# Kernel tuning notes

Measured on AMD Instinct MI355X. Metric: run time of the kernel, lower is better.

## Reference

```python
import jax, jax.numpy as jnp
import numpy as np

W_SIZE = 8
SHIFT = 4
HEADS = 8
EPS = 1e-5


def _layernorm(x, w, b):
    mu = jnp.mean(x, axis=-1, keepdims=True)
    var = jnp.var(x, axis=-1, keepdims=True)
    return (x - mu) * jax.lax.rsqrt(var + EPS) * w + b


def setup_inputs() -> dict:
    key = jax.random.key(0)
    ks = jax.random.split(key, 8)
    B, C, L = 8, 256, 16384
    s = lambda fan: 1.0 / np.sqrt(fan)
    return {
        "x": jax.random.normal(ks[0], (B, C, L), jnp.float32),
        "norm1_w": jnp.ones((C,), jnp.float32),
        "norm1_b": jnp.zeros((C,), jnp.float32),
        "norm2_w": jnp.ones((C,), jnp.float32),
        "norm2_b": jnp.zeros((C,), jnp.float32),
        "qkv_w": jax.random.normal(ks[1], (C, 3 * C), jnp.float32) * s(C),
        "proj_w": jax.random.normal(ks[2], (C, C), jnp.float32) * s(C),
        "proj_b": jnp.zeros((C,), jnp.float32),
        "ff1_w": jax.random.normal(ks[3], (C, 4 * C), jnp.float32) * s(C),
        "ff1_b": jnp.zeros((4 * C,), jnp.float32),
        "ff2_w": jax.random.normal(ks[4], (4 * C, C), jnp.float32) * s(4 * C),
        "ff2_b": jnp.zeros((C,), jnp.float32),
    }


def _window_attn(xt, qkv_w, proj_w, proj_b):
    # xt: (B, L, C); L assumed divisible by W_SIZE (pad path unused for chosen L)
    B, L, C = xt.shape
    W, H = W_SIZE, HEADS
    D = C // H
    scale = D ** (-0.5)
    if SHIFT:
        xt = jnp.roll(xt, -SHIFT, axis=1)
    n_win = L // W
    xw = xt.reshape(B, n_win, W, C)
    qkv = xw @ qkv_w                      # (B, n, W, 3C)
    q, k, v = jnp.split(qkv, 3, axis=-1)
    def heads(t):
        return t.reshape(B, n_win, W, H, D).transpose(0, 1, 3, 2, 4)  # (B,n,H,W,D)
    q, k, v = heads(q), heads(k), heads(v)
    attn = jnp.einsum('bnhid,bnhjd->bnhij', q, k) * scale
    attn = jax.nn.softmax(attn, axis=-1)
    out = jnp.einsum('bnhij,bnhjd->bnhid', attn, v)
    out = out.transpose(0, 1, 3, 2, 4).reshape(B, n_win, W, C)
    out = out @ proj_w + proj_b
    out = out.reshape(B, L, C)
    if SHIFT:
        out = jnp.roll(out, SHIFT, axis=1)
    return out


def reference(x, norm1_w, norm1_b, norm2_w, norm2_b, qkv_w, proj_w, proj_b,
              ff1_w, ff1_b, ff2_w, ff2_b):
    xt = jnp.transpose(x, (0, 2, 1))  # (B, L, C)
    xt = xt + _window_attn(_layernorm(xt, norm1_w, norm1_b), qkv_w, proj_w, proj_b)
    h = jax.nn.gelu(_layernorm(xt, norm2_w, norm2_b) @ ff1_w + ff1_b, approximate=False)
    xt = xt + (h @ ff2_w + ff2_b)
    return jnp.transpose(xt, (0, 2, 1))  # (B, C, L)
```

## Files before the change

kernel.cpp:

```cpp
#include <hip/hip_runtime.h>
#include <hip/hip_bf16.h>

#define C_ 256
#define L_ 16384
#define CL_ (C_*L_)

typedef unsigned int u32;
typedef unsigned short u16;
typedef __bf16 bf16_t;
typedef bf16_t bf16x8 __attribute__((ext_vector_type(8)));
typedef float f32x4 __attribute__((ext_vector_type(4)));

__device__ __forceinline__ float bf2f(u16 v){ return __builtin_bit_cast(float, ((u32)v)<<16); }
__device__ __forceinline__ u16 f2bf(float f){
  bf16_t h = (bf16_t)f;
  return __builtin_bit_cast(u16, h);
}
__device__ __forceinline__ u32 pack2(float a, float b){
  return (u32)f2bf(a) | ((u32)f2bf(b)<<16);
}

#define AST 528
#define HST 272
#define CST 136
#define OST 68

__global__ void wpack_kernel(const float* __restrict__ qkvw, const float* __restrict__ projw,
                             const float* __restrict__ f1w, const float* __restrict__ f2w,
                             u16* __restrict__ pq, u16* __restrict__ pp,
                             u16* __restrict__ p1, u16* __restrict__ p2)
{
  int bid = blockIdx.x, tid = threadIdx.x;
  const float* src; u16* dst; int stride, n, k;
  if (bid < 96){
    int f = bid*256 + tid;
    int l = f & 63, nt = (f>>6) & 15, kk = f>>10;
    int s = kk>>3, ks = kk&7;
    stride = 768; src = qkvw;
    n = s*256 + nt*16 + (l&15);
    k = ks*32 + ((l>>4)<<3);
    dst = pq + (size_t)s*65536 + ((size_t)(ks*16 + nt)*64 + l)*8;
  } else if (bid < 128){
    int f = (bid-96)*256 + tid;
    int l = f & 63, nt = (f>>6) & 15, ks = f>>10;
    stride = 256; src = projw;
    n = nt*16 + (l&15);
    k = ks*32 + ((l>>4)<<3);
    dst = pp + ((size_t)(ks*16 + nt)*64 + l)*8;
  } else if (bid < 256){
    int f = (bid-128)*256 + tid;
    int l = f & 63, nt = (f>>6) & 15, kk = f>>10;
    int c2 = kk>>3, ks = kk&7;
    stride = 1024; src = f1w;
    n = c2*256 + nt*16 + (l&15);
    k = ks*32 + ((l>>4)<<3);
    dst = p1 + (size_t)c2*65536 + ((size_t)(ks*16 + nt)*64 + l)*8;
  } else {
    int f = (bid-256)*256 + tid;
    int l = f & 63, nt = (f>>6) & 15, ks = f>>10;
    stride = 256; src = f2w;
    n = nt*16 + (l&15);
    k = ks*32 + ((l>>4)<<3);
    dst = p2 + ((size_t)(ks*16 + nt)*64 + l)*8;
  }
  u16 v[8];
  #pragma unroll
  for (int j = 0; j < 8; ++j) v[j] = f2bf(src[(size_t)(k+j)*stride + n]);
  uint4 o;
  o.x = (u32)v[0] | ((u32)v[1]<<16);
  o.y = (u32)v[2] | ((u32)v[3]<<16);
  o.z = (u32)v[4] | ((u32)v[5]<<16);
  o.w = (u32)v[6] | ((u32)v[7]<<16);
  *(uint4*)dst = o;
}

__device__ __forceinline__ void gemmP(const u16* Abase, const u16* __restrict__ pk,
                                      int l, int ntb, f32x4 acc[4][2])
{
  const char* ab = (const char*)Abase + (l&15)*AST + ((l>>4)<<4);
  const u16* bp = pk + ((size_t)ntb*64 + l)*8;
  #pragma unroll
  for (int ks = 0; ks < 8; ++ks){
    const u16* bk = bp + (size_t)ks*8192;
    bf16x8 b0 = *(const bf16x8*)(bk);
    bf16x8 b1 = *(const bf16x8*)(bk + 512);
    bf16x8 a[4];
    #pragma unroll
    for (int m = 0; m < 4; ++m)
      a[m] = *(const bf16x8*)(ab + m*(16*AST) + ks*64);
    #pragma unroll
    for (int m = 0; m < 4; ++m){
      acc[m][0] = __builtin_amdgcn_mfma_f32_16x16x32_bf16(a[m], b0, acc[m][0], 0, 0, 0);
      acc[m][1] = __builtin_amdgcn_mfma_f32_16x16x32_bf16(a[m], b1, acc[m][1], 0, 0, 0);
    }
  }
}
#define ZERO_ACC(A) { _Pragma("unroll") for (int m_ = 0; m_ < 4; ++m_){ A[m_][0] = (f32x4){0,0,0,0}; A[m_][1] = (f32x4){0,0,0,0}; } }

__device__ __forceinline__ void gemmP3(const u16* Abase, const u16* __restrict__ pkq,
                                       int l, int ntb,
                                       f32x4 aq[4][2], f32x4 ak[4][2], f32x4 av[4][2])
{
  const char* ab = (const char*)Abase + (l&15)*AST + ((l>>4)<<4);
  const u16* bq = pkq + ((size_t)ntb*64 + l)*8;
  #pragma unroll
  for (int ks = 0; ks < 8; ++ks){
    const u16* bkq = bq + (size_t)ks*8192;
    bf16x8 q0 = *(const bf16x8*)(bkq);
    bf16x8 q1 = *(const bf16x8*)(bkq + 512);
    bf16x8 k0 = *(const bf16x8*)(bkq + 65536);
    bf16x8 k1 = *(const bf16x8*)(bkq + 65536 + 512);
    bf16x8 v0 = *(const bf16x8*)(bkq + 131072);
    bf16x8 v1 = *(const bf16x8*)(bkq + 131072 + 512);
    bf16x8 a[4];
    #pragma unroll
    for (int m = 0; m < 4; ++m)
      a[m] = *(const bf16x8*)(ab + m*(16*AST) + ks*64);
    #pragma unroll
    for (int m = 0; m < 4; ++m){
      aq[m][0] = __builtin_amdgcn_mfma_f32_16x16x32_bf16(a[m], q0, aq[m][0], 0, 0, 0);
      aq[m][1] = __builtin_amdgcn_mfma_f32_16x16x32_bf16(a[m], q1, aq[m][1], 0, 0, 0);
      ak[m][0] = __builtin_amdgcn_mfma_f32_16x16x32_bf16(a[m], k0, ak[m][0], 0, 0, 0);
      ak[m][1] = __builtin_amdgcn_mfma_f32_16x16x32_bf16(a[m], k1, ak[m][1], 0, 0, 0);
      av[m][0] = __builtin_amdgcn_mfma_f32_16x16x32_bf16(a[m], v0, av[m][0], 0, 0, 0);
      av[m][1] = __builtin_amdgcn_mfma_f32_16x16x32_bf16(a[m], v1, av[m][1], 0, 0, 0);
    }
  }
}

__device__ __forceinline__ void gemmF(const u16* Abase, const u16* __restrict__ pk,
                                      int l, int ntb, f32x4 acc[4][2])
{
  #pragma unroll
  for (int ks = 0; ks < 8; ++ks){
    bf16x8 b0 = *(const bf16x8*)(pk + ((size_t)(ks*16 + ntb    )*64 + l)*8);
    bf16x8 b1 = *(const bf16x8*)(pk + ((size_t)(ks*16 + ntb + 1)*64 + l)*8);
    int k0 = ks*32;
    bf16x8 a[4];
    #pragma unroll
    for (int m = 0; m < 4; ++m){
      int t = m*16 + (l & 15);
      int off = t*512 + ((2*(k0 + ((l>>4)<<3))) ^ ((t&7)<<4));
      a[m] = *(const bf16x8*)((const char*)Abase + off);
    }
    #pragma unroll
    for (int m = 0; m < 4; ++m){
      acc[m][0] = __builtin_amdgcn_mfma_f32_16x16x32_bf16(a[m], b0, acc[m][0], 0, 0, 0);
      acc[m][1] = __builtin_amdgcn_mfma_f32_16x16x32_bf16(a[m], b1, acc[m][1], 0, 0, 0);
    }
  }
}

__launch_bounds__(512, 2)
__global__ void swin_attn_kernel(const float* __restrict__ x,
                                 const float* __restrict__ n1w, const float* __restrict__ n1b,
                                 const u16* __restrict__ pkq, const u16* __restrict__ pkp,
                                 const float* __restrict__ projb,
                                 u16* __restrict__ xt1g, float* __restrict__ statsg)
{
  __shared__ char smem[73216];
  u16* Buf1 = (u16*)smem;
  char* Buf2 = smem + 33792;
  float* redF = (float*)(smem + 68608);
  float* statsF = redF + 1024;

  const int tid = threadIdx.x;
  const int w = tid >> 6;
  const int l = tid & 63;
  const int bb = blockIdx.x >> 8;
  const int blkl = blockIdx.x & 255;
  const int l0 = blkl*64 + 4;
  const float* xb = x + (size_t)bb*CL_;
  const int ntb = w*2;

  const int q4 = tid & 15, cg = tid >> 4;
  int lq = l0 + 4*q4; if (lq >= L_) lq -= L_;
  u32 praw[4][4];
  {
    float4 xr[8];
    float s1[4] = {0.f,0.f,0.f,0.f};
    float s2[4] = {0.f,0.f,0.f,0.f};
    #pragma unroll
    for (int ci = 0; ci < 8; ++ci){
      int c = cg*8 + ci;
      float4 d = *(const float4*)(xb + (size_t)c*L_ + lq);
      xr[ci] = d;
      s1[0]+=d.x; s2[0]+=d.x*d.x;  s1[1]+=d.y; s2[1]+=d.y*d.y;
      s1[2]+=d.z; s2[2]+=d.z*d.z;  s1[3]+=d.w; s2[3]+=d.w*d.w;
    }
    #pragma unroll
    for (int off = 16; off < 64; off <<= 1){
      #pragma unroll
      for (int jj = 0; jj < 4; ++jj){
        s1[jj] += __shfl_xor(s1[jj], off);
        s2[jj] += __shfl_xor(s2[jj], off);
      }
    }
    if (l < 16){
      #pragma unroll
      for (int jj = 0; jj < 4; ++jj){
        redF[w*64 + 4*l + jj] = s1[jj];
        redF[512 + w*64 + 4*l + jj] = s2[jj];
      }
    }
    __syncthreads();
    if (tid < 64){
      float a = 0.f, b2 = 0.f;
      #pragma unroll
      for (int ww = 0; ww < 8; ++ww){ a += redF[ww*64 + tid]; b2 += redF[512 + ww*64 + tid]; }
      float mu = a * (1.f/256.f);
      float var = fmaxf(b2 * (1.f/256.f) - mu*mu, 0.f);
      statsF[2*tid] = mu;
      statsF[2*tid+1] = rsqrtf(var + 1e-5f);
    }
    __syncthreads();
    #pragma unroll
    for (int jj = 0; jj < 4; ++jj){
      int t = 4*q4 + jj;
      float mu = statsF[2*t], rs = statsF[2*t+1];
      u32 aw[4];
      #pragma unroll
      for (int cp = 0; cp < 4; ++cp){
        int c0c = cg*8 + 2*cp;
        float v0 = ((const float*)&xr[2*cp])[jj];
        float v1 = ((const float*)&xr[2*cp+1])[jj];
        aw[cp] = pack2((v0-mu)*rs*n1w[c0c] + n1b[c0c], (v1-mu)*rs*n1w[c0c+1] + n1b[c0c+1]);
        praw[jj][cp] = pack2(v0, v1);
      }
      *(uint4*)((char*)Buf1 + t*AST + cg*16) = make_uint4(aw[0],aw[1],aw[2],aw[3]);
    }
  }
  __syncthreads();

  f32x4 aq[4][2], ak[4][2], av[4][2];
  ZERO_ACC(aq); ZERO_ACC(ak); ZERO_ACC(av);
  gemmP3(Buf1, pkq, l, ntb, aq, ak, av);

  #pragma unroll
  for (int m = 0; m < 4; ++m)
    #pragma unroll
    for (int n2 = 0; n2 < 2; ++n2)
      #pragma unroll
      for (int jj = 0; jj < 4; ++jj){
        int t = m*16 + ((l>>4)<<2) + jj;
        int c = (w<<5) + (n2<<4) + (l&15);
        *(u16*)(Buf2 + t*AST + 2*c) = f2bf(ak[m][n2][jj]);
      }
  __syncthreads();

  const int hh = (tid >> 3) & 7, rr = tid & 7;
  const int tq = w*8 + rr;
  u32 kr[16];
  #pragma unroll
  for (int g = 0; g < 4; ++g){
    uint4 dk = *(const uint4*)(Buf2 + tq*AST + hh*64 + 16*g);
    kr[g*4+0] = dk.x; kr[g*4+1] = dk.y; kr[g*4+2] = dk.z; kr[g*4+3] = dk.w;
  }
  __syncthreads();

  #pragma unroll
  for (int m = 0; m < 4; ++m)
    #pragma unroll
    for (int n2 = 0; n2 < 2; ++n2)
      #pragma unroll
      for (int jj = 0; jj < 4; ++jj){
        int t = m*16 + ((l>>4)<<2) + jj;
        int c = (w<<5) + (n2<<4) + (l&15);
        *(u16*)(Buf2 + t*AST + 2*c) = f2bf(aq[m][n2][jj]);
      }
  __syncthreads();

  float pr[8];
  {
    float qf[32];
    #pragma unroll
    for (int g = 0; g < 4; ++g){
      uint4 dq = *(const uint4*)(Buf2 + tq*AST + hh*64 + 16*g);
      qf[g*8+0] = bf2f((u16)dq.x); qf[g*8+1] = bf2f((u16)(dq.x>>16));
      qf[g*8+2] = bf2f((u16)dq.y); qf[g*8+3] = bf2f((u16)(dq.y>>16));
      qf[g*8+4] = bf2f((u16)dq.z); qf[g*8+5] = bf2f((u16)(dq.z>>16));
      qf[g*8+6] = bf2f((u16)dq.w); qf[g*8+7] = bf2f((u16)(dq.w>>16));
    }
    float s[8];
    #pragma unroll
    for (int j = 0; j < 8; ++j){
      float dot = 0.f;
      #pragma unroll
      for (int reg = 0; reg < 16; ++reg){
        u32 kj = (u32)__shfl((int)kr[reg], j, 8);
        dot += qf[2*reg]   * bf2f((u16)kj);
        dot += qf[2*reg+1] * bf2f((u16)(kj>>16));
      }
      s[j] = dot * 0.17677669529663687f;
    }
    float mx = s[0];
    #pragma unroll
    for (int j = 1; j < 8; ++j) mx = fmaxf(mx, s[j]);
    float sum = 0.f;
    #pragma unroll
    for (int j = 0; j < 8; ++j){ pr[j] = __expf(s[j]-mx); sum += pr[j]; }
    float inv = 1.0f / sum;
    #pragma unroll
    for (int j = 0; j < 8; ++j) pr[j] *= inv;
  }
  __syncthreads();

  #pragma unroll
  for (int m = 0; m < 4; ++m)
    #pragma unroll
    for (int n2 = 0; n2 < 2; ++n2)
      #pragma unroll
      for (int jj = 0; jj < 4; ++jj){
        int t = m*16 + ((l>>4)<<2) + jj;
        int c = (w<<5) + (n2<<4) + (l&15);
        *(u16*)(Buf2 + t*AST + 2*c) = f2bf(av[m][n2][jj]);
      }
  #pragma unroll
  for (int jj = 0; jj < 4; ++jj){
    int t = 4*q4 + jj;
    *(uint4*)((char*)Buf1 + t*AST + cg*16) =
        make_uint4(praw[jj][0], praw[jj][1], praw[jj][2], praw[jj][3]);
  }
  __syncthreads();

  {
    u32 vr[16];
    #pragma unroll
    for (int g = 0; g < 4; ++g){
      uint4 dv = *(const uint4*)(Buf2 + tq*AST + hh*64 + 16*g);
      vr[g*4+0] = dv.x; vr[g*4+1] = dv.y; vr[g*4+2] = dv.z; vr[g*4+3] = dv.w;
    }
    float of[32];
    #pragma unroll
    for (int d = 0; d < 32; ++d) of[d] = 0.f;
    #pragma unroll
    for (int j = 0; j < 8; ++j){
      float pj = pr[j];
      #pragma unroll
      for (int reg = 0; reg < 16; ++reg){
        u32 vj = (u32)__shfl((int)vr[reg], j, 8);
        of[2*reg]   += pj*bf2f((u16)vj);
        of[2*reg+1] += pj*bf2f((u16)(vj>>16));
      }
    }
    #pragma unroll
    for (int g = 0; g < 4; ++g){
      uint4 o;
      o.x = pack2(of[g*8+0], of[g*8+1]);
      o.y = pack2(of[g*8+2], of[g*8+3]);
      o.z = pack2(of[g*8+4], of[g*8+5]);
      o.w = pack2(of[g*8+6], of[g*8+7]);
      *(uint4*)(Buf2 + tq*AST + hh*64 + 16*g) = o;
    }
  }
  __syncthreads();

  {
    f32x4 acc[4][2]; ZERO_ACC(acc);
    gemmP((const u16*)Buf2, pkp, l, ntb, acc);
    __syncthreads();
    #pragma unroll
    for (int m = 0; m < 4; ++m)
      #pragma unroll
      for (int n2 = 0; n2 < 2; ++n2)
        #pragma unroll
        for (int jj = 0; jj < 4; ++jj){
          int t = m*16 + ((l>>4)<<2) + jj;
          int c = (w<<5) + (n2<<4) + (l&15);
          float rv = bf2f(*(const u16*)((char*)Buf1 + t*AST + 2*c));
          float v = acc[m][n2][jj] + projb[c] + rv;
          *(u16*)(Buf2 + c*CST + 2*t) = f2bf(v);
        }
  }
  __syncthreads();

  {
    float a = 0.f, b2 = 0.f;
    #pragma unroll
    for (int ci = 0; ci < 32; ++ci){
      int c = (w<<5) + ci;
      float v = bf2f(*(const u16*)(Buf2 + c*CST + 2*l));
      a += v; b2 += v*v;
    }
    redF[w*64 + l] = a;
    redF[512 + w*64 + l] = b2;
  }
  u16* xo = xt1g + (size_t)bb*CL_;
  #pragma unroll
  for (int ii = 0; ii < 8; ++ii){
    int id = tid + ii*512;
    int c = id >> 4, qd = id & 15;
    int lw = l0 + 4*qd; if (lw >= L_) lw -= L_;
    uint2 dd = *(const uint2*)(Buf2 + c*CST + 8*qd);
    *(uint2*)(xo + (size_t)c*L_ + lw) = dd;
  }
  __syncthreads();
  if (tid < 64){
    float a = 0.f, b2 = 0.f;
    #pragma unroll
    for (int ww = 0; ww < 8; ++ww){ a += redF[ww*64 + tid]; b2 += redF[512 + ww*64 + tid]; }
    float mu = a * (1.f/256.f);
    float var = fmaxf(b2 * (1.f/256.f) - mu*mu, 0.f);
    float2 st; st.x = mu; st.y = rsqrtf(var + 1e-5f);
    *(float2*)(statsg + (size_t)(bb*16384 + blkl*64 + tid)*2) = st;
  }
}

__launch_bounds__(512, 4)
__global__ void swin_ff_kernel(const u16* __restrict__ xt1g, const float* __restrict__ statsg,
                               const float* __restrict__ n2w, const float* __restrict__ n2b,
                               const u16* __restrict__ pk1, const float* __restrict__ f1b,
                               const u16* __restrict__ pk2, const float* __restrict__ f2b,
                               float* __restrict__ out)
{
  __shared__ char smem[51200];
  u16* Buf1 = (u16*)smem;
  char* BufH = smem + 33792;

  const int tid = threadIdx.x;
  const int w = tid >> 6;
  const int l = tid & 63;
  const int bb = blockIdx.x >> 8;
  const int blkl = blockIdx.x & 255;
  const int l0 = blkl*64 + 4;
  const u16* xi = xt1g + (size_t)bb*CL_;

  const int q4 = tid & 15, cg = tid >> 4;
  int lq = l0 + 4*q4; if (lq >= L_) lq -= L_;
  {
    u32 xl[8][2];
    #pragma unroll
    for (int ci = 0; ci < 8; ++ci){
      int c = cg*8 + ci;
      uint2 dd = *(const uint2*)(xi + (size_t)c*L_ + lq);
      xl[ci][0] = dd.x; xl[ci][1] = dd.y;
    }
    #pragma unroll
    for (int jj = 0; jj < 4; ++jj){
      int t = 4*q4 + jj;
      float2 st = *(const float2*)(statsg + (size_t)(bb*16384 + blkl*64 + t)*2);
      float mu = st.x, rs = st.y;
      u32 aw[4];
      #pragma unroll
      for (int cp = 0; cp < 4; ++cp){
        int c0c = cg*8 + 2*cp;
        float v0 = bf2f((u16)(xl[2*cp  ][jj>>1] >> (16*(jj&1))));
        float v1 = bf2f((u16)(xl[2*cp+1][jj>>1] >> (16*(jj&1))));
        aw[cp] = pack2((v0-mu)*rs*n2w[c0c] + n2b[c0c], (v1-mu)*rs*n2w[c0c+1] + n2b[c0c+1]);
      }
      *(uint4*)((char*)Buf1 + t*AST + cg*16) = make_uint4(aw[0],aw[1],aw[2],aw[3]);
    }
  }
  __syncthreads();

  f32x4 acc2[4][2]; ZERO_ACC(acc2);
  const char* ab1 = (const char*)Buf1 + (l&15)*AST + ((l>>4)<<4);
  const char* abh = BufH + (l&15)*HST + ((l>>4)<<4);
  #pragma unroll 1
  for (int j = 0; j < 8; ++j){
    f32x4 acc1[4];
    #pragma unroll
    for (int m = 0; m < 4; ++m) acc1[m] = (f32x4){0,0,0,0};
    const u16* p1 = pk1 + (size_t)(j>>1)*65536;
    const int ntf = ((j&1)<<3) + w;
    const u16* bp1 = p1 + ((size_t)ntf*64 + l)*8;
    #pragma unroll
    for (int ks = 0; ks < 8; ++ks){
      bf16x8 b = *(const bf16x8*)(bp1 + (size_t)ks*8192);
      #pragma unroll
      for (int m = 0; m < 4; ++m){
        bf16x8 a = *(const bf16x8*)(ab1 + m*(16*AST) + ks*64);
        acc1[m] = __builtin_amdgcn_mfma_f32_16x16x32_bf16(a, b, acc1[m], 0, 0, 0);
      }
    }
    __syncthreads();
    #pragma unroll
    for (int m = 0; m < 4; ++m)
      #pragma unroll
      for (int jj = 0; jj < 4; ++jj){
        int t = m*16 + ((l>>4)<<2) + jj;
        int cp_ = (w<<4) + (l&15);
        float xv = acc1[m][jj] + f1b[j*128 + cp_];
        float u = xv*(0.79788456f + 0.035677408f*xv*xv);
        float g = xv / (1.f + __expf(-2.f*u));
        *(u16*)(BufH + t*HST + 2*cp_) = f2bf(g);
      }
    __syncthreads();
    const u16* bp2 = pk2 + ((size_t)(4*j*16 + 2*w)*64 + l)*8;
    #pragma unroll
    for (int ks2 = 0; ks2 < 4; ++ks2){
      const u16* bk = bp2 + (size_t)ks2*8192;
      bf16x8 b0 = *(const bf16x8*)(bk);
      bf16x8 b1 = *(const bf16x8*)(bk + 512);
      bf16x8 a[4];
      #pragma unroll
      for (int m = 0; m < 4; ++m)
        a[m] = *(const bf16x8*)(abh + m*(16*HST) + ks2*64);
      #pragma unroll
      for (int m = 0; m < 4; ++m){
        acc2[m][0] = __builtin_amdgcn_mfma_f32_16x16x32_bf16(a[m], b0, acc2[m][0], 0, 0, 0);
        acc2[m][1] = __builtin_amdgcn_mfma_f32_16x16x32_bf16(a[m], b1, acc2[m][1], 0, 0, 0);
      }
    }
  }

  float* OutF = (float*)smem;
  float* ob = out + (size_t)bb*CL_;
  #pragma unroll
  for (int n2p = 0; n2p < 2; ++n2p){
    __syncthreads();
    #pragma unroll
    for (int m = 0; m < 4; ++m)
      #pragma unroll
      for (int jj = 0; jj < 4; ++jj){
        int t = m*16 + ((l>>4)<<2) + jj;
        int c = (w<<5) + (n2p<<4) + (l&15);
        int row = (w<<4) + (l&15);
        float v = acc2[m][n2p][jj] + f2b[c];
        OutF[row*OST + t] = v;
      }
    __syncthreads();
    #pragma unroll
    for (int ii = 0; ii < 4; ++ii){
      int id = tid + ii*512;
      int row = id >> 4, qd = id & 15;
      int cg_ = ((row>>4)<<5) + (n2p<<4) + (row&15);
      int lw = l0 + 4*qd; if (lw >= L_) lw -= L_;
      float4 vv = *(const float4*)(OutF + row*OST + 4*qd);
      uint2 rr2 = *(const uint2*)(xi + (size_t)cg_*L_ + lw);
      vv.x += bf2f((u16)rr2.x);  vv.y += bf2f((u16)(rr2.x>>16));
      vv.z += bf2f((u16)rr2.y);  vv.w += bf2f((u16)(rr2.y>>16));
      *(float4*)(ob + (size_t)cg_*L_ + lw) = vv;
    }
  }
}

__launch_bounds__(512, 2)
__global__ void swin_fused_kernel(const float* __restrict__ x,
                                  const float* __restrict__ n1w, const float* __restrict__ n1b,
                                  const float* __restrict__ n2w, const float* __restrict__ n2b,
                                  const u16* __restrict__ pkq, const u16* __restrict__ pkp,
                                  const float* __restrict__ projb,
                                  const u16* __restrict__ pk1, const float* __restrict__ f1b,
                                  const u16* __restrict__ pk2, const float* __restrict__ f2b,
                                  float* __restrict__ out)
{
  __shared__ u16 smem[35072];
  u16* Buf1 = smem;
  u16* Buf2 = smem + 16384;
  float* redF   = (float*)(smem + 32768);
  float* statsF = redF + 1024;

  const int tid = threadIdx.x;
  const int w = tid >> 6;
  const int l = tid & 63;
  const int bb = blockIdx.x >> 8;
  const int blkl = blockIdx.x & 255;
  const int l0 = blkl*64 + 4;
  const float* xb = x + (size_t)bb*CL_;
  const int ntb = w*2;

  const int q4 = tid & 15, cg = tid >> 4;
  int lq = l0 + 4*q4; if (lq >= L_) lq -= L_;
  float4 xr[8];
  float s1[4] = {0.f,0.f,0.f,0.f};
  float s2[4] = {0.f,0.f,0.f,0.f};
  #pragma unroll
  for (int ci = 0; ci < 8; ++ci){
    int c = cg*8 + ci;
    float4 d = *(const float4*)(xb + (size_t)c*L_ + lq);
    xr[ci] = d;
    s1[0]+=d.x; s2[0]+=d.x*d.x;  s1[1]+=d.y; s2[1]+=d.y*d.y;
    s1[2]+=d.z; s2[2]+=d.z*d.z;  s1[3]+=d.w; s2[3]+=d.w*d.w;
  }
  #pragma unroll
  for (int off = 16; off < 64; off <<= 1){
    #pragma unroll
    for (int jj = 0; jj < 4; ++jj){
      s1[jj] += __shfl_xor(s1[jj], off);
      s2[jj] += __shfl_xor(s2[jj], off);
    }
  }
  if (l < 16){
    #pragma unroll
    for (int jj = 0; jj < 4; ++jj){
      redF[w*64 + 4*l + jj] = s1[jj];
      redF[512 + w*64 + 4*l + jj] = s2[jj];
    }
  }
  __syncthreads();
  if (tid < 64){
    float a = 0.f, b2 = 0.f;
    #pragma unroll
    for (int ww = 0; ww < 8; ++ww){ a += redF[ww*64 + tid]; b2 += redF[512 + ww*64 + tid]; }
    float mu = a * (1.f/256.f);
    float var = fmaxf(b2 * (1.f/256.f) - mu*mu, 0.f);
    statsF[2*tid] = mu;
    statsF[2*tid+1] = rsqrtf(var + 1e-5f);
  }
  __syncthreads();

  u32 praw[4][4];
  #pragma unroll
  for (int jj = 0; jj < 4; ++jj){
    int t = 4*q4 + jj;
    float mu = statsF[2*t], rs = statsF[2*t+1];
    u32 aw[4];
    #pragma unroll
    for (int cp = 0; cp < 4; ++cp){
      int c0c = cg*8 + 2*cp;
      float v0 = ((const float*)&xr[2*cp])[jj];
      float v1 = ((const float*)&xr[2*cp+1])[jj];
      aw[cp] = pack2((v0-mu)*rs*n1w[c0c] + n1b[c0c], (v1-mu)*rs*n1w[c0c+1] + n1b[c0c+1]);
      praw[jj][cp] = pack2(v0, v1);
    }
    *(uint4*)((char*)Buf1 + t*512 + ((cg*16) ^ ((t&7)<<4))) = make_uint4(aw[0],aw[1],aw[2],aw[3]);
  }
  __syncthreads();

  {
    f32x4 acc[4][2]; ZERO_ACC(acc);
    gemmF(Buf1, pkq + 65536, l, ntb, acc);
    #pragma unroll
    for (int m = 0; m < 4; ++m)
      #pragma unroll
      for (int n2 = 0; n2 < 2; ++n2)
        #pragma unroll
        for (int jj = 0; jj < 4; ++jj){
          int t = m*16 + ((l>>4)<<2) + jj;
          int c = (w<<5) + (n2<<4) + (l&15);
          *(u16*)((char*)Buf2 + t*512 + ((2*c) ^ ((t&7)<<4))) = f2bf(acc[m][n2][jj]);
        }
  }
  __syncthreads();

  const int hh = (tid >> 3) & 7, rr = tid & 7;
  const int tq = w*8 + rr;
  u32 kr[16];
  #pragma unroll
  for (int g = 0; g < 4; ++g){
    uint4 dk = *(const uint4*)((char*)Buf2 + tq*512 + ((hh*64 + 16*g) ^ ((tq&7)<<4)));
    kr[g*4+0] = dk.x; kr[g*4+1] = dk.y; kr[g*4+2] = dk.z; kr[g*4+3] = dk.w;
  }
  __syncthreads();

  {
    f32x4 acc[4][2]; ZERO_ACC(acc);
    gemmF(Buf1, pkq, l, ntb, acc);
    #pragma unroll
    for (int m = 0; m < 4; ++m)
      #pragma unroll
      for (int n2 = 0; n2 < 2; ++n2)
        #pragma unroll
        for (int jj = 0; jj < 4; ++jj){
          int t = m*16 + ((l>>4)<<2) + jj;
          int c = (w<<5) + (n2<<4) + (l&15);
          *(u16*)((char*)Buf2 + t*512 + ((2*c) ^ ((t&7)<<4))) = f2bf(acc[m][n2][jj]);
        }
  }
  __syncthreads();

  float pr[8];
  {
    float qf[32];
    #pragma unroll
    for (int g = 0; g < 4; ++g){
      uint4 dq = *(const uint4*)((char*)Buf2 + tq*512 + ((hh*64 + 16*g) ^ ((tq&7)<<4)));
      qf[g*8+0] = bf2f((u16)dq.x); qf[g*8+1] = bf2f((u16)(dq.x>>16));
      qf[g*8+2] = bf2f((u16)dq.y); qf[g*8+3] = bf2f((u16)(dq.y>>16));
      qf[g*8+4] = bf2f((u16)dq.z); qf[g*8+5] = bf2f((u16)(dq.z>>16));
      qf[g*8+6] = bf2f((u16)dq.w); qf[g*8+7] = bf2f((u16)(dq.w>>16));
    }
    float s[8];
    #pragma unroll
    for (int j = 0; j < 8; ++j){
      float dot = 0.f;
      #pragma unroll
      for (int reg = 0; reg < 16; ++reg){
        u32 kj = (u32)__shfl((int)kr[reg], j, 8);
        dot += qf[2*reg]   * bf2f((u16)kj);
        dot += qf[2*reg+1] * bf2f((u16)(kj>>16));
      }
      s[j] = dot * 0.17677669529663687f;
    }
    float mx = s[0];
    #pragma unroll
    for (int j = 1; j < 8; ++j) mx = fmaxf(mx, s[j]);
    float sum = 0.f;
    #pragma unroll
    for (int j = 0; j < 8; ++j){ pr[j] = __expf(s[j]-mx); sum += pr[j]; }
    float inv = 1.0f / sum;
    #pragma unroll
    for (int j = 0; j < 8; ++j) pr[j] *= inv;
  }
  __syncthreads();

  {
    f32x4 acc[4][2]; ZERO_ACC(acc);
    gemmF(Buf1, pkq + 131072, l, ntb, acc);
    __syncthreads();
    #pragma unroll
    for (int m = 0; m < 4; ++m)
      #pragma unroll
      for (int n2 = 0; n2 < 2; ++n2)
        #pragma unroll
        for (int jj = 0; jj < 4; ++jj){
          int t = m*16 + ((l>>4)<<2) + jj;
          int c = (w<<5) + (n2<<4) + (l&15);
          *(u16*)((char*)Buf2 + t*512 + ((2*c) ^ ((t&7)<<4))) = f2bf(acc[m][n2][jj]);
        }
    #pragma unroll
    for (int jj = 0; jj < 4; ++jj){
      int t = 4*q4 + jj;
      *(uint4*)((char*)Buf1 + t*512 + ((cg*16) ^ ((t&7)<<4))) =
          make_uint4(praw[jj][0], praw[jj][1], praw[jj][2], praw[jj][3]);
    }
  }
  __syncthreads();

  {
    u32 vr[16];
    #pragma unroll
    for (int g = 0; g < 4; ++g){
      uint4 dv = *(const uint4*)((char*)Buf2 + tq*512 + ((hh*64 + 16*g) ^ ((tq&7)<<4)));
      vr[g*4+0] = dv.x; vr[g*4+1] = dv.y; vr[g*4+2] = dv.z; vr[g*4+3] = dv.w;
    }
    float of[32];
    #pragma unroll
    for (int d = 0; d < 32; ++d) of[d] = 0.f;
    #pragma unroll
    for (int j = 0; j < 8; ++j){
      float pj = pr[j];
      #pragma unroll
      for (int reg = 0; reg < 16; ++reg){
        u32 vj = (u32)__shfl((int)vr[reg], j, 8);
        of[2*reg]   += pj*bf2f((u16)vj);
        of[2*reg+1] += pj*bf2f((u16)(vj>>16));
      }
    }
    #pragma unroll
    for (int g = 0; g < 4; ++g){
      uint4 o;
      o.x = pack2(of[g*8+0], of[g*8+1]);
      o.y = pack2(of[g*8+2], of[g*8+3]);
      o.z = pack2(of[g*8+4], of[g*8+5]);
      o.w = pack2(of[g*8+6], of[g*8+7]);
      *(uint4*)((char*)Buf2 + tq*512 + ((hh*64 + 16*g) ^ ((tq&7)<<4))) = o;
    }
  }
  __syncthreads();

  u32 xt1p[4][2][2];
  {
    f32x4 acc[4][2]; ZERO_ACC(acc);
    gemmF(Buf2, pkp, l, ntb, acc);
    __syncthreads();
    #pragma unroll
    for (int m = 0; m < 4; ++m)
      #pragma unroll
      for (int n2 = 0; n2 < 2; ++n2){
        float vv[4];
        #pragma unroll
        for (int jj = 0; jj < 4; ++jj){
          int t = m*16 + ((l>>4)<<2) + jj;
          int c = (w<<5) + (n2<<4) + (l&15);
          float rv = bf2f(*(const u16*)((char*)Buf1 + t*512 + ((2*c) ^ ((t&7)<<4))));
          float v = acc[m][n2][jj] + projb[c] + rv;
          vv[jj] = v;
          *(u16*)((char*)Buf2 + t*512 + 2*c) = f2bf(v);
        }
        xt1p[m][n2][0] = pack2(vv[0], vv[1]);
        xt1p[m][n2][1] = pack2(vv[2], vv[3]);
      }
  }
  __syncthreads();

  {
    float4 wv = *(const float4*)(n2w + 4*l);
    float4 bv = *(const float4*)(n2b + 4*l);
    #pragma unroll 1
    for (int r = 0; r < 8; ++r){
      int t = w*8 + r;
      uint2 d = *(const uint2*)((char*)Buf2 + t*512 + 8*l);
      float f0 = bf2f((u16)d.x), f1 = bf2f((u16)(d.x>>16));
      float f2 = bf2f((u16)d.y), f3 = bf2f((u16)(d.y>>16));
      float ls1 = f0+f1+f2+f3;
      float ls2 = f0*f0+f1*f1+f2*f2+f3*f3;
      #pragma unroll
      for (int off = 1; off < 64; off <<= 1){
        ls1 += __shfl_xor(ls1, off);
        ls2 += __shfl_xor(ls2, off);
      }
      float mu = ls1 * (1.f/256.f);
      float var = fmaxf(ls2 * (1.f/256.f) - mu*mu, 0.f);
      float rs = rsqrtf(var + 1e-5f);
      uint2 pp;
      pp.x = pack2((f0-mu)*rs*wv.x+bv.x, (f1-mu)*rs*wv.y+bv.y);
      pp.y = pack2((f2-mu)*rs*wv.z+bv.z, (f3-mu)*rs*wv.w+bv.w);
      *(uint2*)((char*)Buf1 + t*512 + ((8*l) ^ ((t&7)<<4))) = pp;
    }
  }
  __syncthreads();

  f32x4 acc2[4][2]; ZERO_ACC(acc2);
  #pragma unroll 1
  for (int c2 = 0; c2 < 4; ++c2){
    f32x4 acc1[4][2]; ZERO_ACC(acc1);
    gemmF(Buf1, pk1 + (size_t)c2*65536, l, ntb, acc1);
    __syncthreads();
    #pragma unroll
    for (int m = 0; m < 4; ++m)
      #pragma unroll
      for (int n2 = 0; n2 < 2; ++n2)
        #pragma unroll
        for (int jj = 0; jj < 4; ++jj){
          int t = m*16 + ((l>>4)<<2) + jj;
          int c = (w<<5) + (n2<<4) + (l&15);
          float xv = acc1[m][n2][jj] + f1b[c2*256 + c];
          float u = xv*(0.79788456f + 0.035677408f*xv*xv);
          float g = xv / (1.f + __expf(-2.f*u));
          *(u16*)((char*)Buf2 + t*512 + ((2*c) ^ ((t&7)<<4))) = f2bf(g);
        }
    __syncthreads();
    gemmF(Buf2, pk2 + (size_t)c2*65536, l, ntb, acc2);
    __syncthreads();
  }

  float* OutF = (float*)smem;
  #pragma unroll
  for (int m = 0; m < 4; ++m)
    #pragma unroll
    for (int n2 = 0; n2 < 2; ++n2)
      #pragma unroll
      for (int jj = 0; jj < 4; ++jj){
        int t = m*16 + ((l>>4)<<2) + jj;
        int c = (w<<5) + (n2<<4) + (l&15);
        u32 p = xt1p[m][n2][jj>>1];
        float rv = bf2f((u16)((jj&1) ? (p>>16) : (p&0xFFFF)));
        float v = acc2[m][n2][jj] + f2b[c] + rv;
        *(float*)((char*)OutF + c*256 + ((4*t) ^ ((c&15)<<4))) = v;
      }
  __syncthreads();

  float* ob = out + (size_t)bb*CL_;
  #pragma unroll
  for (int ii = 0; ii < 8; ++ii){
    int id = tid + ii*512;
    int c = id >> 4, qd = id & 15;
    int lw = l0 + 4*qd; if (lw >= L_) lw -= L_;
    float4 vv = *(const float4*)((char*)OutF + c*256 + ((16*qd) ^ ((c&15)<<4)));
    *(float4*)(ob + (size_t)c*L_ + lw) = vv;
  }
}

extern "C" void kernel_launch(void* const* d_in, const int* in_sizes, int n_in,
                              void* d_out, int out_size, void* d_ws, size_t ws_size,
                              hipStream_t stream)
{
  const float* x     = (const float*)d_in[0];
  const float* n1w   = (const float*)d_in[1];
  const float* n1b   = (const float*)d_in[2];
  const float* n2w   = (const float*)d_in[3];
  const float* n2b   = (const float*)d_in[4];
  const float* qkvw  = (const float*)d_in[5];
  const float* projw = (const float*)d_in[6];
  const float* projb = (const float*)d_in[7];
  const float* f1w   = (const float*)d_in[8];
  const float* f1b   = (const float*)d_in[9];
  const float* f2w   = (const float*)d_in[10];
  const float* f2b   = (const float*)d_in[11];
  float* out = (float*)d_out;

  u16* ws  = (u16*)d_ws;
  u16* pkq = ws;
  u16* pkp = pkq + 196608;
  u16* pk1 = pkp + 65536;
  u16* pk2 = pk1 + 262144;
  u16* xt1g = pk2 + 262144;
  float* statsg = (float*)(xt1g + (size_t)8*CL_);

  size_t need = (size_t)786432*2 + (size_t)8*CL_*2 + (size_t)8*16384*2*4;

  hipLaunchKernelGGL(wpack_kernel, dim3(384), dim3(256), 0, stream,
                     qkvw, projw, f1w, f2w, pkq, pkp, pk1, pk2);
  if (ws_size >= need){
    hipLaunchKernelGGL(swin_attn_kernel, dim3(2048), dim3(512), 0, stream,
                       x, n1w, n1b, pkq, pkp, projb, xt1g, statsg);
    hipLaunchKernelGGL(swin_ff_kernel, dim3(2048), dim3(512), 0, stream,
                       xt1g, statsg, n2w, n2b, pk1, f1b, pk2, f2b, out);
  } else {
    hipLaunchKernelGGL(swin_fused_kernel, dim3(2048), dim3(512), 0, stream,
                       x, n1w, n1b, n2w, n2b, pkq, pkp, projb, pk1, f1b, pk2, f2b, out);
  }
}
```

Baseline: 427.9 us.

## Process two FF1 hidden chunks per iteration with double hidden buffer

The FF kernel loop now computes two 128-wide slices of the hidden layer per iteration into two separate LDS buffers, then runs the FF2 accumulation over both. This halves the number of loop iterations and barriers, and gives the scheduler two independent MFMA chains to interleave. In exchange, shared memory grows from about 50KB to 67KB per block and more accumulator registers are live, which may reduce occupancy below the launch-bounds target of 4 blocks.

Measured after the change: 419.6 us. No clear change (-1.9%).

```diff
diff --git a/kernel.cpp b/kernel.cpp
--- a/kernel.cpp
+++ b/kernel.cpp
@@ -413,9 +413,10 @@
                                const u16* __restrict__ pk2, const float* __restrict__ f2b,
                                float* __restrict__ out)
 {
-  __shared__ char smem[51200];
-  u16* Buf1 = (u16*)smem;
-  char* BufH = smem + 33792;
+  __shared__ char smem[68608];
+  u16* Buf1  = (u16*)smem;
+  char* BufH0 = smem + 33792;
+  char* BufH1 = smem + 51200;
 
   const int tid = threadIdx.x;
   const int w = tid >> 6;
@@ -455,53 +456,59 @@
 
   f32x4 acc2[4][2]; ZERO_ACC(acc2);
   const char* ab1 = (const char*)Buf1 + (l&15)*AST + ((l>>4)<<4);
-  const char* abh = BufH + (l&15)*HST + ((l>>4)<<4);
   #pragma unroll 1
-  for (int j = 0; j < 8; ++j){
-    f32x4 acc1[4];
-    #pragma unroll
-    for (int m = 0; m < 4; ++m) acc1[m] = (f32x4){0,0,0,0};
-    const u16* p1 = pk1 + (size_t)(j>>1)*65536;
-    const int ntf = ((j&1)<<3) + w;
-    const u16* bp1 = p1 + ((size_t)ntf*64 + l)*8;
+  for (int jp = 0; jp < 4; ++jp){
+    f32x4 a1a[4], a1b[4];
+    #pragma unroll
+    for (int m = 0; m < 4; ++m){ a1a[m] = (f32x4){0,0,0,0}; a1b[m] = (f32x4){0,0,0,0}; }
+    const u16* p1 = pk1 + (size_t)jp*65536;
+    const u16* bpA = p1 + ((size_t)(w    )*64 + l)*8;
+    const u16* bpB = p1 + ((size_t)(8 + w)*64 + l)*8;
     #pragma unroll
     for (int ks = 0; ks < 8; ++ks){
-      bf16x8 b = *(const bf16x8*)(bp1 + (size_t)ks*8192);
+      bf16x8 bA = *(const bf16x8*)(bpA + (size_t)ks*8192);
+      bf16x8 bB = *(const bf16x8*)(bpB + (size_t)ks*8192);
       #pragma unroll
       for (int m = 0; m < 4; ++m){
         bf16x8 a = *(const bf16x8*)(ab1 + m*(16*AST) + ks*64);
-        acc1[m] = __builtin_amdgcn_mfma_f32_16x16x32_bf16(a, b, acc1[m], 0, 0, 0);
-      }
-    }
-    __syncthreads();
+        a1a[m] = __builtin_amdgcn_mfma_f32_16x16x32_bf16(a, bA, a1a[m], 0, 0, 0);
+        a1b[m] = __builtin_amdgcn_mfma_f32_16x16x32_bf16(a, bB, a1b[m], 0, 0, 0);
+      }
+    }
     #pragma unroll
     for (int m = 0; m < 4; ++m)
       #pragma unroll
       for (int jj = 0; jj < 4; ++jj){
         int t = m*16 + ((l>>4)<<2) + jj;
         int cp_ = (w<<4) + (l&15);
-        float xv = acc1[m][jj] + f1b[j*128 + cp_];
-        float u = xv*(0.79788456f + 0.035677408f*xv*xv);
-        float g = xv / (1.f + __expf(-2.f*u));
-        *(u16*)(BufH + t*HST + 2*cp_) = f2bf(g);
-      }
-    __syncthreads();
-    const u16* bp2 = pk2 + ((size_t)(4*j*16 + 2*w)*64 + l)*8;
-    #pragma unroll
-    for (int ks2 = 0; ks2 < 4; ++ks2){
-      const u16* bk = bp2 + (size_t)ks2*8192;
+        float xa = a1a[m][jj] + f1b[(2*jp)*128 + cp_];
+        float ua = xa*(0.79788456f + 0.035677408f*xa*xa);
+        *(u16*)(BufH0 + t*HST + 2*cp_) = f2bf(xa / (1.f + __expf(-2.f*ua)));
+        float xb = a1b[m][jj] + f1b[(2*jp+1)*128 + cp_];
+        float ub = xb*(0.79788456f + 0.035677408f*xb*xb);
+        *(u16*)(BufH1 + t*HST + 2*cp_) = f2bf(xb / (1.f + __expf(-2.f*ub)));
+      }
+    __syncthreads();
+    const u16* bp2 = pk2 + ((size_t)((8*jp)*16 + 2*w)*64 + l)*8;
+    #pragma unroll
+    for (int kk = 0; kk < 8; ++kk){
+      const char* hb = (kk < 4) ? BufH0 : BufH1;
+      const char* abh = hb + (l&15)*HST + ((l>>4)<<4);
+      int ksl = kk & 3;
+      const u16* bk = bp2 + (size_t)kk*8192;
       bf16x8 b0 = *(const bf16x8*)(bk);
       bf16x8 b1 = *(const bf16x8*)(bk + 512);
       bf16x8 a[4];
       #pragma unroll
       for (int m = 0; m < 4; ++m)
-        a[m] = *(const bf16x8*)(abh + m*(16*HST) + ks2*64);
+        a[m] = *(const bf16x8*)(abh + m*(16*HST) + ksl*64);
       #pragma unroll
       for (int m = 0; m < 4; ++m){
         acc2[m][0] = __builtin_amdgcn_mfma_f32_16x16x32_bf16(a[m], b0, acc2[m][0], 0, 0, 0);
         acc2[m][1] = __builtin_amdgcn_mfma_f32_16x16x32_bf16(a[m], b1, acc2[m][1], 0, 0, 0);
       }
     }
+    __syncthreads();
   }
 
   float* OutF = (float*)smem;
```
